# Optimization experiments

Measured on AMD Instinct MI355X. Metric: run time of the kernel, lower is better.

## Reference

```python
import jax, jax.numpy as jnp
import numpy as np

B, A, HR = 2, 180, 512
H_OUT = W_OUT = 512


def setup_inputs() -> dict:
    key = jax.random.key(0)
    k1, = jax.random.split(key, 1)
    sino = jax.random.normal(k1, (B, A, HR), dtype=jnp.float32)
    angles_deg = jnp.linspace(0.0, 180.0, A, endpoint=False, dtype=jnp.float32)
    return {"sino": sino, "angles_deg": angles_deg, "H": H_OUT, "W": W_OUT}


def _forward(sino, angles_deg, H, W):
    Bn, An, Hr = sino.shape
    pad = int(1.0 * 0.1 * min(H, W))  # pad_ratio = 1.0
    Hp, Wp = H + 2 * pad, W + 2 * pad

    # --- F.interpolate bilinear, align_corners=False: (A,B,Hr,1) -> (A,B,Hp,Wp).
    # Input width is 1, so width interp replicates the single column; only height interp matters.
    src = jnp.clip((jnp.arange(Hp, dtype=jnp.float32) + 0.5) * (Hr / Hp) - 0.5, 0.0, Hr - 1)
    i0 = jnp.floor(src).astype(jnp.int32)
    i1 = jnp.minimum(i0 + 1, Hr - 1)
    wH = src - i0.astype(jnp.float32)
    p = jnp.transpose(sino, (1, 0, 2)).astype(jnp.float32)  # (A,B,Hr)
    col = p[:, :, i0] * (1.0 - wH) + p[:, :, i1] * wH       # (A,B,Hp)
    proj = jnp.broadcast_to(col[:, :, :, None], (An, Bn, Hp, Wp))  # (A,B,Hp,Wp)

    # --- affine_grid (align_corners=False), sign = -1
    th = -jnp.deg2rad(angles_deg)
    c, s = jnp.cos(th), jnp.sin(th)                          # (A,)
    xs = (jnp.arange(Wp, dtype=jnp.float32) + 0.5) * (2.0 / Wp) - 1.0
    ys = (jnp.arange(Hp, dtype=jnp.float32) + 0.5) * (2.0 / Hp) - 1.0
    gx = c[:, None, None] * xs[None, None, :] - s[:, None, None] * ys[None, :, None]  # (A,Hp,Wp)
    gy = s[:, None, None] * xs[None, None, :] + c[:, None, None] * ys[None, :, None]

    # --- grid_sample bilinear, zeros padding, align_corners=False
    ix = ((gx + 1.0) * Wp - 1.0) * 0.5
    iy = ((gy + 1.0) * Hp - 1.0) * 0.5
    x0 = jnp.floor(ix).astype(jnp.int32); x1 = x0 + 1
    y0 = jnp.floor(iy).astype(jnp.int32); y1 = y0 + 1
    wx = ix - x0.astype(jnp.float32)
    wy = iy - y0.astype(jnp.float32)

    def corner(img, xi, yi, w):  # img (B,Hp,Wp); idx/w (Hp,Wp)
        valid = (xi >= 0) & (xi <= Wp - 1) & (yi >= 0) & (yi <= Hp - 1)
        xc = jnp.clip(xi, 0, Wp - 1)
        yc = jnp.clip(yi, 0, Hp - 1)
        return img[:, yc, xc] * (w * valid.astype(jnp.float32))[None]

    def sample(img, x0a, x1a, y0a, y1a, wxa, wya):
        return (corner(img, x0a, y0a, (1 - wxa) * (1 - wya)) +
                corner(img, x1a, y0a, wxa * (1 - wya)) +
                corner(img, x0a, y1a, (1 - wxa) * wya) +
                corner(img, x1a, y1a, wxa * wya))

    xr = jax.vmap(sample)(proj, x0, x1, y0, y1, wx, wy)      # (A,B,Hp,Wp)
    acc = xr.sum(axis=0) / (An + 1e-06)                      # (B,Hp,Wp)
    acc = acc[:, None, :, :]                                 # (B,1,Hp,Wp)
    if pad > 0:
        acc = acc[:, :, pad:Hp - pad, pad:Wp - pad]
    return acc


def reference(sino, angles_deg, H, W):
    return _forward(sino, angles_deg, H, W)
```

## Files before the change

kernel.cpp:

```cpp
#include <hip/hip_runtime.h>
#include <hip/hip_fp16.h>
#include <math.h>

#define B_N   2
#define A_N   180
#define HR_N  512
#define H_OUT 512
#define W_OUT 512
#define PAD   51
#define HP    614
#define WP    614
#define GUARD 80
#define HPP   (HP + 2*GUARD)
#define NPIX  (H_OUT * W_OUT)

#define TW     16
#define TH     8
#define HALF_A 90
#define CH     30
#define NCH    (HALF_A / CH)
#define WIN    20


__device__ __forceinline__ float col_val(const float* __restrict__ sino,
                                         int b, int a, int yy) {
    if (yy < 0 || yy >= HP) return 0.0f;
    float src = ((float)yy + 0.5f) * ((float)HR_N / (float)HP) - 0.5f;
    src = fminf(fmaxf(src, 0.0f), (float)(HR_N - 1));
    int i0 = (int)floorf(src);
    int i1 = min(i0 + 1, HR_N - 1);
    float wH = src - (float)i0;
    const float* srow = sino + ((size_t)b * A_N + a) * HR_N;
    return srow[i0] * (1.0f - wH) + srow[i1] * wH;
}

__global__ void prep_kernel(const float* __restrict__ sino,
                            const float* __restrict__ angles,
                            uint2* __restrict__ pk2,
                            float2* __restrict__ tg) {
    int idx = blockIdx.x * blockDim.x + threadIdx.x;
    if (idx < A_N) {
        float th = -angles[idx] * (float)(M_PI / 180.0);
        tg[idx] = make_float2(cosf(th), sinf(th));
    }
    const int total = A_N * HPP;
    if (idx < total) {
        int y = idx % HPP;
        int a = idx / HPP;
        int yy = y - GUARD;
        float v00 = col_val(sino, 0, a, yy);
        float v10 = col_val(sino, 1, a, yy);
        float v01 = col_val(sino, 0, a, yy + 1);
        float v11 = col_val(sino, 1, a, yy + 1);
        __half2 lo = __floats2half2_rn(v00, v10);
        __half2 hi = __floats2half2_rn(v01, v11);
        uint2 u;
        u.x = *(unsigned int*)&lo;
        u.y = *(unsigned int*)&hi;
        pk2[idx] = u;
    }
}

__global__ __launch_bounds__(256, 8) void bp_kernel(const uint2* __restrict__ pk2,
                                                    const float2* __restrict__ tgv,
                                                    float* __restrict__ out) {
    __shared__ float4 s_ang[A_N];
    __shared__ int    s_base[A_N];
    __shared__ uint2  s_win[2 * CH * WIN];
    __shared__ float  s_red[2][128];

    int t  = threadIdx.x;
    int tx = blockIdx.x, ty = blockIdx.y;
    float Xc = (float)(tx * TW) - 248.0f;
    float Yc = (float)(ty * TH) - 252.0f;

    if (t < A_N) {
        float2 cs = tgv[t];
        float iyc = fmaf(cs.y, Xc, fmaf(cs.x, Yc, 306.5f));
        int base = (int)floorf(iyc) - 9;
        s_ang[t]  = make_float4(cs.x, cs.y, 306.5f - (float)base, 0.0f);
        s_base[t] = base;
    }

    int half = t >> 7;
    int tt   = t & 127;
    int lx = tt & (TW - 1), ly = tt >> 4;
    float X = (float)(tx * TW + lx) - 255.5f;
    float Y = (float)(ty * TH + ly) - 255.5f;

    float acc0 = 0.0f, acc1 = 0.0f;
    __syncthreads();

    bool interior = (Xc * Xc + Yc * Yc) <= 87500.0f;

    for (int ch = 0; ch < NCH; ++ch) {
        for (int e = t; e < 2 * CH * WIN; e += 256) {
            int hh = e / (CH * WIN);
            int r  = e - hh * (CH * WIN);
            int la = r / WIN;
            int j  = r - la * WIN;
            int a  = hh * HALF_A + ch * CH + la;
            s_win[e] = pk2[(size_t)a * HPP + (GUARD + s_base[a] + j)];
        }
        __syncthreads();

        const int aoff = half * HALF_A + ch * CH;
        const int woff = half * (CH * WIN);
        if (interior) {
#pragma unroll 5
            for (int la = 0; la < CH; ++la) {
                float4 ang = s_ang[aoff + la];
                float f  = fmaf(ang.y, X, fmaf(ang.x, Y, ang.z));
                int   li = (int)f;
                float wy = f - (float)li;
                uint2 cv = s_win[woff + la * WIN + li];
                __half2 lo = *(__half2*)&cv.x;
                __half2 hi = *(__half2*)&cv.y;
                __half2 d  = __hsub2(hi, lo);
                __half2 wv = __float2half2_rn(wy);
                __half2 r2 = __hfma2(wv, d, lo);
                acc0 += __low2float(r2);
                acc1 += __high2float(r2);
            }
        } else {
#pragma unroll 5
            for (int la = 0; la < CH; ++la) {
                float4 ang = s_ang[aoff + la];
                float f  = fmaf(ang.y, X, fmaf(ang.x, Y, ang.z));
                int   li = (int)f;
                float wy = f - (float)li;
                uint2 cv = s_win[woff + la * WIN + li];
                __half2 lo = *(__half2*)&cv.x;
                __half2 hi = *(__half2*)&cv.y;
                __half2 d  = __hsub2(hi, lo);
                __half2 wv = __float2half2_rn(wy);
                __half2 r2 = __hfma2(wv, d, lo);
                float ix = fmaf(ang.x, X, fmaf(-ang.y, Y, 306.5f));
                float xf = fminf(fmaxf(ix + 1.0f, 0.0f), 1.0f)
                         * fminf(fmaxf((float)WP - ix, 0.0f), 1.0f);
                acc0 = fmaf(xf, __low2float(r2), acc0);
                acc1 = fmaf(xf, __high2float(r2), acc1);
            }
        }
        __syncthreads();
    }

    if (half) {
        s_red[0][tt] = acc0;
        s_red[1][tt] = acc1;
    }
    __syncthreads();
    if (!half) {
        const float inv = 1.0f / (180.0f + 1e-6f);
        float a0 = (acc0 + s_red[0][tt]) * inv;
        float a1 = (acc1 + s_red[1][tt]) * inv;
        int idx = (ty * TH + ly) * W_OUT + (tx * TW + lx);
        out[idx]        = a0;
        out[NPIX + idx] = a1;
    }
}

extern "C" void kernel_launch(void* const* d_in, const int* in_sizes, int n_in,
                              void* d_out, int out_size, void* d_ws, size_t ws_size,
                              hipStream_t stream) {
    const float* sino   = (const float*)d_in[0];
    const float* angles = (const float*)d_in[1];
    char*   ws  = (char*)d_ws;
    uint2*  pk2 = (uint2*)ws;
    float2* tg  = (float2*)(ws + (size_t)A_N * HPP * sizeof(uint2));

    const int total = A_N * HPP;
    prep_kernel<<<(total + 255) / 256, 256, 0, stream>>>(sino, angles, pk2, tg);

    dim3 grid(W_OUT / TW, H_OUT / TH);
    bp_kernel<<<grid, 256, 0, stream>>>(pk2, tg, (float*)d_out);
}
```

Measured before the change: 84.67 us.

## Accumulate interior chunks in half2 and recompute angle constants from global

Drops the shared-memory per-angle float4 table. Each thread now reloads cos/sin from global memory (uniform across the block, so likely scalar loads) and recomputes the window offset inline. In the interior path it also accumulates 30 angles per chunk in a packed half2 register before converting to float. Both loops are fully unrolled. The aim is to cut LDS traffic and the per-sample float conversions, at the cost of reduced accumulation precision in fp16 and extra ALU work for the offset recomputation.

```diff
diff --git a/kernel.cpp b/kernel.cpp
--- a/kernel.cpp
+++ b/kernel.cpp
@@ -64,10 +64,9 @@
 __global__ __launch_bounds__(256, 8) void bp_kernel(const uint2* __restrict__ pk2,
                                                     const float2* __restrict__ tgv,
                                                     float* __restrict__ out) {
-    __shared__ float4 s_ang[A_N];
-    __shared__ int    s_base[A_N];
-    __shared__ uint2  s_win[2 * CH * WIN];
-    __shared__ float  s_red[2][128];
+    __shared__ int   s_base[A_N];
+    __shared__ uint2 s_win[2 * CH * WIN];
+    __shared__ float s_red[2][128];
 
     int t  = threadIdx.x;
     int tx = blockIdx.x, ty = blockIdx.y;
@@ -77,9 +76,7 @@
     if (t < A_N) {
         float2 cs = tgv[t];
         float iyc = fmaf(cs.y, Xc, fmaf(cs.x, Yc, 306.5f));
-        int base = (int)floorf(iyc) - 9;
-        s_ang[t]  = make_float4(cs.x, cs.y, 306.5f - (float)base, 0.0f);
-        s_base[t] = base;
+        s_base[t] = (int)floorf(iyc) - 9;
     }
 
     int half = t >> 7;
@@ -107,35 +104,39 @@
         const int aoff = half * HALF_A + ch * CH;
         const int woff = half * (CH * WIN);
         if (interior) {
-#pragma unroll 5
+            __half2 hacc = __float2half2_rn(0.0f);
+#pragma unroll
             for (int la = 0; la < CH; ++la) {
-                float4 ang = s_ang[aoff + la];
-                float f  = fmaf(ang.y, X, fmaf(ang.x, Y, ang.z));
-                int   li = (int)f;
-                float wy = f - (float)li;
-                uint2 cv = s_win[woff + la * WIN + li];
+                float2 cs = tgv[aoff + la];
+                float c = cs.x, s = cs.y;
+                float iyc = fmaf(s, Xc, fmaf(c, Yc, 306.5f));
+                float Kf  = 315.5f - floorf(iyc);
+                float f   = fmaf(s, X, fmaf(c, Y, Kf));
+                int   li  = (int)f;
+                float wy  = f - (float)li;
+                uint2 cv  = s_win[woff + la * WIN + li];
                 __half2 lo = *(__half2*)&cv.x;
                 __half2 hi = *(__half2*)&cv.y;
-                __half2 d  = __hsub2(hi, lo);
-                __half2 wv = __float2half2_rn(wy);
-                __half2 r2 = __hfma2(wv, d, lo);
-                acc0 += __low2float(r2);
-                acc1 += __high2float(r2);
+                __half2 r2 = __hfma2(__float2half2_rn(wy), __hsub2(hi, lo), lo);
+                hacc = __hadd2(hacc, r2);
             }
+            acc0 += __low2float(hacc);
+            acc1 += __high2float(hacc);
         } else {
-#pragma unroll 5
+#pragma unroll
             for (int la = 0; la < CH; ++la) {
-                float4 ang = s_ang[aoff + la];
-                float f  = fmaf(ang.y, X, fmaf(ang.x, Y, ang.z));
-                int   li = (int)f;
-                float wy = f - (float)li;
-                uint2 cv = s_win[woff + la * WIN + li];
+                float2 cs = tgv[aoff + la];
+                float c = cs.x, s = cs.y;
+                float iyc = fmaf(s, Xc, fmaf(c, Yc, 306.5f));
+                float Kf  = 315.5f - floorf(iyc);
+                float f   = fmaf(s, X, fmaf(c, Y, Kf));
+                int   li  = (int)f;
+                float wy  = f - (float)li;
+                uint2 cv  = s_win[woff + la * WIN + li];
                 __half2 lo = *(__half2*)&cv.x;
                 __half2 hi = *(__half2*)&cv.y;
-                __half2 d  = __hsub2(hi, lo);
-                __half2 wv = __float2half2_rn(wy);
-                __half2 r2 = __hfma2(wv, d, lo);
-                float ix = fmaf(ang.x, X, fmaf(-ang.y, Y, 306.5f));
+                __half2 r2 = __hfma2(__float2half2_rn(wy), __hsub2(hi, lo), lo);
+                float ix = fmaf(c, X, fmaf(-s, Y, 306.5f));
                 float xf = fminf(fmaxf(ix + 1.0f, 0.0f), 1.0f)
                          * fminf(fmaxf((float)WP - ix, 0.0f), 1.0f);
                 acc0 = fmaf(xf, __low2float(r2), acc0);
```

Measured after the change: 86.66 us. 2.3% more time.
